# Performance work log

Hardware: AMD Instinct MI355X
Metric: run time of the kernel (lower is better)

The kernel has to match this reference:

```python
import jax, jax.numpy as jnp
import numpy as np

K_VALUES = (2, 4, 8)  # sorted k_values from init


def setup_inputs() -> dict:
    key = jax.random.key(0)
    ks = jax.random.split(key, 6)
    B, T, D, H = 16, 2048, 512, 64
    nk = len(K_VALUES)
    # columns: (E, Pt, eta, phi) -- E,Pt positive, eta in [-3,3], phi in [-pi,pi]
    u = jax.random.uniform(ks[0], (B, T, 4), jnp.float32)
    tokens_cont = u * jnp.array([100.0, 50.0, 6.0, 6.2832], jnp.float32) + jnp.array([1.0, 1.0, -3.0, -3.1416], jnp.float32)
    lengths = jax.random.randint(ks[1], (B,), T // 2, T + 1)
    mask = jnp.arange(T)[None, :] < lengths[:, None]  # [B,T] True=valid
    W1 = jax.random.normal(ks[2], (nk, H), jnp.float32) / np.sqrt(nk).astype(np.float32)
    b1 = jax.random.normal(ks[3], (H,), jnp.float32) * 0.01
    W2 = jax.random.normal(ks[4], (H, D), jnp.float32) / np.sqrt(H).astype(np.float32)
    b2 = jax.random.normal(ks[5], (D,), jnp.float32) * 0.01
    return dict(tokens_cont=tokens_cont, mask=mask, W1=W1, b1=b1, W2=W2, b2=b2)


def reference(tokens_cont, mask, W1, b1, W2, b2):
    B, T, _ = tokens_cont.shape
    E, Pt, eta, phi = (tokens_cont[..., i] for i in range(4))
    px = Pt * jnp.cos(phi)
    py = Pt * jnp.sin(phi)
    pz = Pt * jnp.sinh(jnp.clip(eta, -20.0, 20.0))
    P = jnp.stack([E, px, py, pz], axis=-1)  # [B,T,4] four-momentum
    metric = jnp.array([1.0, -1.0, -1.0, -1.0], P.dtype)
    # Lorentz dot: E_i E_j - px_i px_j - py_i py_j - pz_i pz_j -> [B,T,T]
    dot = jnp.einsum('btc,bsc->bts', P * metric, P)
    dot = jnp.where(mask[:, None, :], dot, -jnp.inf)  # exclude padding friends
    max_k = min(max(K_VALUES), T)
    _, topk_idx = jax.lax.top_k(dot, max_k)  # [B,T,max_k]
    Pf = P[jnp.arange(B)[:, None, None], topk_idx]  # gather friends [B,T,max_k,4]
    cum = jnp.cumsum(Pf, axis=2)  # prefix sums over sorted friends
    masses = []
    maskf = mask.astype(P.dtype)
    for k in K_VALUES:
        ps = cum[:, :, min(k, max_k) - 1, :]  # [B,T,4] summed 4-momentum of top-k group
        m2 = ps[..., 0] ** 2 - jnp.sum(ps[..., 1:] ** 2, axis=-1)
        m2 = jnp.maximum(m2, 0.0) * maskf
        masses.append(jnp.sqrt(m2 + 1e-8))
    mass = jnp.stack(masses, axis=-1)  # [B,T,n_k]
    h = jax.nn.gelu(mass @ W1 + b1, approximate=False)  # torch GELU = exact erf
    return h @ W2 + b2  # [B,T,model_dim]
```

## Files before the change

### kernel.cpp

```cpp
#include <hip/hip_runtime.h>
#include <hip/hip_bf16.h>
#include <math.h>

#define NB 16
#define NT 2048
#define ND 512
#define NH 64

typedef __attribute__((ext_vector_type(8))) short short8;
typedef __attribute__((ext_vector_type(4))) float float4v;

__device__ __forceinline__ bool mask_is_bytes(const int* m) {
    return m[0] == 0x01010101;
}
__device__ __forceinline__ bool mask_at(const int* m, bool bytes, int i) {
    if (bytes) return ((const unsigned char*)m)[i] != 0;
    return m[i] != 0;
}

__device__ __forceinline__ float dot4(float4 a, float4 p) {
    float d = a.x * p.x;
    d = __builtin_fmaf(a.y, p.y, d);
    d = __builtin_fmaf(a.z, p.z, d);
    d = __builtin_fmaf(a.w, p.w, d);
    return d;
}

__device__ __forceinline__ unsigned short f2bf(float x) {
    unsigned int u = __float_as_uint(x);
    u += 0x7fffu + ((u >> 16) & 1u);
    return (unsigned short)(u >> 16);
}

__global__ void __launch_bounds__(256) w2t_kernel(
        const float* __restrict__ W2, unsigned short* __restrict__ W2t) {
    int i = blockIdx.x * 256 + threadIdx.x;
    int n = i & (ND - 1), k = i >> 9;
    W2t[n * NH + k] = f2bf(W2[k * ND + n]);
}

#define VT(w2, j, l)  scratch[((w2) * 8 + (j)) * 64 + (l)]
#define PS(w2, c, l)  scratch[((w2) * 12 + (c)) * 64 + (l)]

__global__ void __launch_bounds__(512) fused_topk_mass_mlp_kernel(
        const float* __restrict__ tok,
        const int* __restrict__ mask,
        const float* __restrict__ W1,
        const float* __restrict__ b1,
        const unsigned short* __restrict__ W2t,
        const float* __restrict__ b2,
        float* __restrict__ out) {
    __shared__ float Plds[NT * 4];
    __shared__ float scratch[8 * 12 * 64];
    __shared__ unsigned short hs[64][88];
    __shared__ float mass_s[3][64];
    __shared__ int wcnt[8];

    const int b    = blockIdx.y;
    const int t0   = blockIdx.x * 64;
    const int tid  = threadIdx.x;
    const int lane = tid & 63;
    const int w    = tid >> 6;
    const bool mb  = mask_is_bytes(mask);

    const bool blockValid = mask_at(mask, mb, b * NT + t0);

    if (blockValid) {
        int cnt = 0;
#pragma unroll
        for (int it = 0; it < 4; ++it) {
            int i = tid + it * 512;
            float4 tv = ((const float4*)tok)[b * NT + i];
            bool m = mask_at(mask, mb, b * NT + i);
            float E = tv.x, Pt = tv.y, eta = tv.z, phi = tv.w;
            float px = Pt * cosf(phi);
            float py = Pt * sinf(phi);
            float pz = Pt * sinhf(fminf(fmaxf(eta, -20.f), 20.f));
            float4 pv = m ? make_float4(E, px, py, pz)
                          : make_float4(-1e30f, 0.f, 0.f, 0.f);
            *(float4*)&Plds[i * 4] = pv;
            cnt += (int)__popcll(__ballot(m));
        }
        if (lane == 0) wcnt[w] = cnt;
        __syncthreads();

        int L = 0;
#pragma unroll
        for (int j = 0; j < 8; ++j) L += wcnt[j];
        const int C    = (L + 7) >> 3;
        const int sBeg = w * C;
        const int sEnd = min(sBeg + C, L);

        float4 pt = *(const float4*)&Plds[(t0 + lane) * 4];
        float4 a  = make_float4(pt.x, -pt.y, -pt.z, -pt.w);

        const float NEGBIG = -3.402823466e38f;
        float v0 = NEGBIG, v1 = NEGBIG, v2 = NEGBIG, v3 = NEGBIG;
        float v4 = NEGBIG, v5 = NEGBIG, v6 = NEGBIG, v7 = NEGBIG;

#pragma unroll 4
        for (int s = sBeg; s < sEnd; ++s) {
            float4 ps = *(const float4*)&Plds[s * 4];
            float d = dot4(a, ps);
            float n0 = fmaxf(v0, d);
            float n1 = __builtin_amdgcn_fmed3f(d, v0, v1);
            float n2 = __builtin_amdgcn_fmed3f(d, v1, v2);
            float n3 = __builtin_amdgcn_fmed3f(d, v2, v3);
            float n4 = __builtin_amdgcn_fmed3f(d, v3, v4);
            float n5 = __builtin_amdgcn_fmed3f(d, v4, v5);
            float n6 = __builtin_amdgcn_fmed3f(d, v5, v6);
            float n7 = __builtin_amdgcn_fmed3f(d, v6, v7);
            v0 = n0; v1 = n1; v2 = n2; v3 = n3;
            v4 = n4; v5 = n5; v6 = n6; v7 = n7;
        }
        VT(w, 0, lane) = v0; VT(w, 1, lane) = v1;
        VT(w, 2, lane) = v2; VT(w, 3, lane) = v3;
        VT(w, 4, lane) = v4; VT(w, 5, lane) = v5;
        VT(w, 6, lane) = v6; VT(w, 7, lane) = v7;
        __syncthreads();

        float m0 = NEGBIG, m1 = NEGBIG, m2_ = NEGBIG, m3 = NEGBIG;
        float m4 = NEGBIG, m5 = NEGBIG, m6 = NEGBIG, m7 = NEGBIG;
#pragma unroll
        for (int w2 = 0; w2 < 8; ++w2) {
#pragma unroll
            for (int j = 0; j < 8; ++j) {
                float d = VT(w2, j, lane);
                float n0 = fmaxf(m0, d);
                float n1 = __builtin_amdgcn_fmed3f(d, m0, m1);
                float n2 = __builtin_amdgcn_fmed3f(d, m1, m2_);
                float n3 = __builtin_amdgcn_fmed3f(d, m2_, m3);
                float n4 = __builtin_amdgcn_fmed3f(d, m3, m4);
                float n5 = __builtin_amdgcn_fmed3f(d, m4, m5);
                float n6 = __builtin_amdgcn_fmed3f(d, m5, m6);
                float n7 = __builtin_amdgcn_fmed3f(d, m6, m7);
                m0 = n0; m1 = n1; m2_ = n2; m3 = n3;
                m4 = n4; m5 = n5; m6 = n6; m7 = n7;
            }
        }
        const float th2 = m1, th4 = m3, th8 = m7;
        __syncthreads();

        float s2x = 0.f, s2y = 0.f, s2z = 0.f, s2w = 0.f;
        float s4x = 0.f, s4y = 0.f, s4z = 0.f, s4w = 0.f;
        float s8x = 0.f, s8y = 0.f, s8z = 0.f, s8w = 0.f;
#pragma unroll 4
        for (int s = sBeg; s < sEnd; ++s) {
            float4 ps = *(const float4*)&Plds[s * 4];
            float d = dot4(a, ps);
            if (d >= th8) {
                s8x += ps.x; s8y += ps.y; s8z += ps.z; s8w += ps.w;
                if (d >= th4) {
                    s4x += ps.x; s4y += ps.y; s4z += ps.z; s4w += ps.w;
                    if (d >= th2) {
                        s2x += ps.x; s2y += ps.y; s2z += ps.z; s2w += ps.w;
                    }
                }
            }
        }
        PS(w, 0, lane) = s2x;  PS(w, 1, lane) = s2y;
        PS(w, 2, lane) = s2z;  PS(w, 3, lane) = s2w;
        PS(w, 4, lane) = s4x;  PS(w, 5, lane) = s4y;
        PS(w, 6, lane) = s4z;  PS(w, 7, lane) = s4w;
        PS(w, 8, lane) = s8x;  PS(w, 9, lane) = s8y;
        PS(w, 10, lane) = s8z; PS(w, 11, lane) = s8w;
        __syncthreads();

        if (w == 0) {
            float tot[12];
#pragma unroll
            for (int c = 0; c < 12; ++c) {
                float acc = 0.f;
#pragma unroll
                for (int w2 = 0; w2 < 8; ++w2) acc += PS(w2, c, lane);
                tot[c] = acc;
            }
            const bool maskt = (t0 + lane) < L;
            const float MZ = sqrtf(1e-8f);
            auto massf = [&](float sx, float sy, float sz, float sw) -> float {
                float q = sx * sx;
                q = __builtin_fmaf(-sy, sy, q);
                q = __builtin_fmaf(-sz, sz, q);
                q = __builtin_fmaf(-sw, sw, q);
                q = fmaxf(q, 0.f);
                return sqrtf(q + 1e-8f);
            };
            mass_s[0][lane] = maskt ? massf(tot[0], tot[1], tot[2], tot[3]) : MZ;
            mass_s[1][lane] = maskt ? massf(tot[4], tot[5], tot[6], tot[7]) : MZ;
            mass_s[2][lane] = maskt ? massf(tot[8], tot[9], tot[10], tot[11]) : MZ;
        }
    } else {
        if (tid < 64) {
            const float MZ = sqrtf(1e-8f);
            mass_s[0][tid] = MZ;
            mass_s[1][tid] = MZ;
            mass_s[2][tid] = MZ;
        }
    }
    __syncthreads();

    {
        const int tt = lane;
        const int hr = w;
        float q0 = mass_s[0][tt];
        float q1 = mass_s[1][tt];
        float q2 = mass_s[2][tt];
        unsigned short hv[8];
#pragma unroll
        for (int j = 0; j < 8; ++j) {
            int hh = hr * 8 + j;
            float pre = b1[hh];
            pre = __builtin_fmaf(q0, W1[hh], pre);
            pre = __builtin_fmaf(q1, W1[NH + hh], pre);
            pre = __builtin_fmaf(q2, W1[2 * NH + hh], pre);
            float g = 0.5f * pre * (1.0f + erff(pre * 0.70710678118654752f));
            hv[j] = f2bf(g);
        }
        *(short8*)&hs[tt][hr * 8] = *(const short8*)hv;
    }
    __syncthreads();

    const int col   = lane & 15;
    const int quad  = lane >> 4;
    const int mhalf = w >> 2;
    const int nBase = (w & 3) * 128;

    short8 afrag[2][2];
#pragma unroll
    for (int mt = 0; mt < 2; ++mt)
#pragma unroll
        for (int ks = 0; ks < 2; ++ks)
            afrag[mt][ks] = *(const short8*)&hs[mhalf * 32 + mt * 16 + col][ks * 32 + quad * 8];

    float4v acc[2][8];
#pragma unroll
    for (int mt = 0; mt < 2; ++mt)
#pragma unroll
        for (int nt = 0; nt < 8; ++nt)
            acc[mt][nt] = (float4v)(0.f);

#pragma unroll
    for (int nt = 0; nt < 8; ++nt) {
        const unsigned short* wp = W2t + (nBase + nt * 16 + col) * NH + quad * 8;
        short8 bf0 = *(const short8*)(wp);
        short8 bf1 = *(const short8*)(wp + 32);
        acc[0][nt] = __builtin_amdgcn_mfma_f32_16x16x32_bf16(afrag[0][0], bf0, acc[0][nt], 0, 0, 0);
        acc[1][nt] = __builtin_amdgcn_mfma_f32_16x16x32_bf16(afrag[1][0], bf0, acc[1][nt], 0, 0, 0);
        acc[0][nt] = __builtin_amdgcn_mfma_f32_16x16x32_bf16(afrag[0][1], bf1, acc[0][nt], 0, 0, 0);
        acc[1][nt] = __builtin_amdgcn_mfma_f32_16x16x32_bf16(afrag[1][1], bf1, acc[1][nt], 0, 0, 0);
    }

#pragma unroll
    for (int nt = 0; nt < 8; ++nt) {
        float bias = b2[nBase + nt * 16 + col];
#pragma unroll
        for (int mt = 0; mt < 2; ++mt) {
            int mRow = b * NT + t0 + mhalf * 32 + mt * 16 + quad * 4;
            size_t base = (size_t)mRow * ND + nBase + nt * 16 + col;
#pragma unroll
            for (int r = 0; r < 4; ++r) {
                out[base + (size_t)r * ND] = acc[mt][nt][r] + bias;
            }
        }
    }
}

extern "C" void kernel_launch(void* const* d_in, const int* in_sizes, int n_in,
                              void* d_out, int out_size, void* d_ws, size_t ws_size,
                              hipStream_t stream) {
    const float* tok  = (const float*)d_in[0];
    const int*   mask = (const int*)d_in[1];
    const float* W1   = (const float*)d_in[2];
    const float* b1   = (const float*)d_in[3];
    const float* W2   = (const float*)d_in[4];
    const float* b2   = (const float*)d_in[5];
    float*       out  = (float*)d_out;

    unsigned short* W2t = (unsigned short*)d_ws;

    w2t_kernel<<<dim3(ND * NH / 256), dim3(256), 0, stream>>>(W2, W2t);

    dim3 gB(NT / 64, NB);
    fused_topk_mass_mlp_kernel<<<gB, dim3(512), 0, stream>>>(
        tok, mask, W1, b1, W2t, b2, out);
}
```

Before: 133.6 us.

## Process two query tiles per block to reuse LDS friend loads

Each block now handles 128 query tokens instead of 64, so every lane tracks two top-8 lists and two sets of prefix sums. Each LDS load of a friend four-momentum is shared by two dot products. This halves the grid and the per-block preamble work (computing P for all 2048 tokens, mask popcounts). The cost is more register pressure from doubled accumulators, a larger LDS scratch buffer, and fewer blocks, which may lower occupancy and parallelism. The MLP stage runs twice per block.

After: 148.7 us. +11.3%, slower.

```diff
diff --git a/kernel.cpp b/kernel.cpp
--- a/kernel.cpp
+++ b/kernel.cpp
@@ -32,6 +32,20 @@
     return (unsigned short)(u >> 16);
 }
 
+#define INS8(V0,V1,V2,V3,V4,V5,V6,V7,D)                          \
+    {                                                            \
+        float n0 = fmaxf(V0, D);                                 \
+        float n1 = __builtin_amdgcn_fmed3f(D, V0, V1);           \
+        float n2 = __builtin_amdgcn_fmed3f(D, V1, V2);           \
+        float n3 = __builtin_amdgcn_fmed3f(D, V2, V3);           \
+        float n4 = __builtin_amdgcn_fmed3f(D, V3, V4);           \
+        float n5 = __builtin_amdgcn_fmed3f(D, V4, V5);           \
+        float n6 = __builtin_amdgcn_fmed3f(D, V5, V6);           \
+        float n7 = __builtin_amdgcn_fmed3f(D, V6, V7);           \
+        V0 = n0; V1 = n1; V2 = n2; V3 = n3;                      \
+        V4 = n4; V5 = n5; V6 = n6; V7 = n7;                      \
+    }
+
 __global__ void __launch_bounds__(256) w2t_kernel(
         const float* __restrict__ W2, unsigned short* __restrict__ W2t) {
     int i = blockIdx.x * 256 + threadIdx.x;
@@ -39,8 +53,8 @@
     W2t[n * NH + k] = f2bf(W2[k * ND + n]);
 }
 
-#define VT(w2, j, l)  scratch[((w2) * 8 + (j)) * 64 + (l)]
-#define PS(w2, c, l)  scratch[((w2) * 12 + (c)) * 64 + (l)]
+#define VT(w2, j, l)  scratch[((w2) * 8 + (j)) * 128 + (l)]
+#define PS(w2, c, l)  scratch[((w2) * 12 + (c)) * 128 + (l)]
 
 __global__ void __launch_bounds__(512) fused_topk_mass_mlp_kernel(
         const float* __restrict__ tok,
@@ -51,13 +65,13 @@
         const float* __restrict__ b2,
         float* __restrict__ out) {
     __shared__ float Plds[NT * 4];
-    __shared__ float scratch[8 * 12 * 64];
+    __shared__ float scratch[8 * 12 * 128];
     __shared__ unsigned short hs[64][88];
-    __shared__ float mass_s[3][64];
+    __shared__ float mass_s[3][128];
     __shared__ int wcnt[8];
 
     const int b    = blockIdx.y;
-    const int t0   = blockIdx.x * 64;
+    const int t0   = blockIdx.x * 128;
     const int tid  = threadIdx.x;
     const int lane = tid & 63;
     const int w    = tid >> 6;
@@ -91,91 +105,108 @@
         const int sBeg = w * C;
         const int sEnd = min(sBeg + C, L);
 
-        float4 pt = *(const float4*)&Plds[(t0 + lane) * 4];
-        float4 a  = make_float4(pt.x, -pt.y, -pt.z, -pt.w);
+        float4 ptA = *(const float4*)&Plds[(t0 + lane) * 4];
+        float4 ptB = *(const float4*)&Plds[(t0 + 64 + lane) * 4];
+        float4 aA  = make_float4(ptA.x, -ptA.y, -ptA.z, -ptA.w);
+        float4 aB  = make_float4(ptB.x, -ptB.y, -ptB.z, -ptB.w);
 
         const float NEGBIG = -3.402823466e38f;
-        float v0 = NEGBIG, v1 = NEGBIG, v2 = NEGBIG, v3 = NEGBIG;
-        float v4 = NEGBIG, v5 = NEGBIG, v6 = NEGBIG, v7 = NEGBIG;
+        float A0 = NEGBIG, A1 = NEGBIG, A2 = NEGBIG, A3 = NEGBIG;
+        float A4 = NEGBIG, A5 = NEGBIG, A6 = NEGBIG, A7 = NEGBIG;
+        float B0 = NEGBIG, B1 = NEGBIG, B2 = NEGBIG, B3 = NEGBIG;
+        float B4 = NEGBIG, B5 = NEGBIG, B6 = NEGBIG, B7 = NEGBIG;
 
 #pragma unroll 4
         for (int s = sBeg; s < sEnd; ++s) {
             float4 ps = *(const float4*)&Plds[s * 4];
-            float d = dot4(a, ps);
-            float n0 = fmaxf(v0, d);
-            float n1 = __builtin_amdgcn_fmed3f(d, v0, v1);
-            float n2 = __builtin_amdgcn_fmed3f(d, v1, v2);
-            float n3 = __builtin_amdgcn_fmed3f(d, v2, v3);
-            float n4 = __builtin_amdgcn_fmed3f(d, v3, v4);
-            float n5 = __builtin_amdgcn_fmed3f(d, v4, v5);
-            float n6 = __builtin_amdgcn_fmed3f(d, v5, v6);
-            float n7 = __builtin_amdgcn_fmed3f(d, v6, v7);
-            v0 = n0; v1 = n1; v2 = n2; v3 = n3;
-            v4 = n4; v5 = n5; v6 = n6; v7 = n7;
-        }
-        VT(w, 0, lane) = v0; VT(w, 1, lane) = v1;
-        VT(w, 2, lane) = v2; VT(w, 3, lane) = v3;
-        VT(w, 4, lane) = v4; VT(w, 5, lane) = v5;
-        VT(w, 6, lane) = v6; VT(w, 7, lane) = v7;
-        __syncthreads();
-
-        float m0 = NEGBIG, m1 = NEGBIG, m2_ = NEGBIG, m3 = NEGBIG;
-        float m4 = NEGBIG, m5 = NEGBIG, m6 = NEGBIG, m7 = NEGBIG;
+            float dA = dot4(aA, ps);
+            float dB = dot4(aB, ps);
+            INS8(A0, A1, A2, A3, A4, A5, A6, A7, dA);
+            INS8(B0, B1, B2, B3, B4, B5, B6, B7, dB);
+        }
+        VT(w, 0, lane) = A0; VT(w, 1, lane) = A1;
+        VT(w, 2, lane) = A2; VT(w, 3, lane) = A3;
+        VT(w, 4, lane) = A4; VT(w, 5, lane) = A5;
+        VT(w, 6, lane) = A6; VT(w, 7, lane) = A7;
+        VT(w, 0, 64 + lane) = B0; VT(w, 1, 64 + lane) = B1;
+        VT(w, 2, 64 + lane) = B2; VT(w, 3, 64 + lane) = B3;
+        VT(w, 4, 64 + lane) = B4; VT(w, 5, 64 + lane) = B5;
+        VT(w, 6, 64 + lane) = B6; VT(w, 7, 64 + lane) = B7;
+        __syncthreads();
+
+        float mA0 = NEGBIG, mA1 = NEGBIG, mA2 = NEGBIG, mA3 = NEGBIG;
+        float mA4 = NEGBIG, mA5 = NEGBIG, mA6 = NEGBIG, mA7 = NEGBIG;
+        float mB0 = NEGBIG, mB1 = NEGBIG, mB2 = NEGBIG, mB3 = NEGBIG;
+        float mB4 = NEGBIG, mB5 = NEGBIG, mB6 = NEGBIG, mB7 = NEGBIG;
 #pragma unroll
         for (int w2 = 0; w2 < 8; ++w2) {
 #pragma unroll
             for (int j = 0; j < 8; ++j) {
-                float d = VT(w2, j, lane);
-                float n0 = fmaxf(m0, d);
-                float n1 = __builtin_amdgcn_fmed3f(d, m0, m1);
-                float n2 = __builtin_amdgcn_fmed3f(d, m1, m2_);
-                float n3 = __builtin_amdgcn_fmed3f(d, m2_, m3);
-                float n4 = __builtin_amdgcn_fmed3f(d, m3, m4);
-                float n5 = __builtin_amdgcn_fmed3f(d, m4, m5);
-                float n6 = __builtin_amdgcn_fmed3f(d, m5, m6);
-                float n7 = __builtin_amdgcn_fmed3f(d, m6, m7);
-                m0 = n0; m1 = n1; m2_ = n2; m3 = n3;
-                m4 = n4; m5 = n5; m6 = n6; m7 = n7;
-            }
-        }
-        const float th2 = m1, th4 = m3, th8 = m7;
-        __syncthreads();
-
-        float s2x = 0.f, s2y = 0.f, s2z = 0.f, s2w = 0.f;
-        float s4x = 0.f, s4y = 0.f, s4z = 0.f, s4w = 0.f;
-        float s8x = 0.f, s8y = 0.f, s8z = 0.f, s8w = 0.f;
+                float dA = VT(w2, j, lane);
+                float dB = VT(w2, j, 64 + lane);
+                INS8(mA0, mA1, mA2, mA3, mA4, mA5, mA6, mA7, dA);
+                INS8(mB0, mB1, mB2, mB3, mB4, mB5, mB6, mB7, dB);
+            }
+        }
+        const float th2A = mA1, th4A = mA3, th8A = mA7;
+        const float th2B = mB1, th4B = mB3, th8B = mB7;
+        __syncthreads();
+
+        float a2x = 0.f, a2y = 0.f, a2z = 0.f, a2w = 0.f;
+        float a4x = 0.f, a4y = 0.f, a4z = 0.f, a4w = 0.f;
+        float a8x = 0.f, a8y = 0.f, a8z = 0.f, a8w = 0.f;
+        float b2x = 0.f, b2y = 0.f, b2z = 0.f, b2w = 0.f;
+        float b4x = 0.f, b4y = 0.f, b4z = 0.f, b4w = 0.f;
+        float b8x = 0.f, b8y = 0.f, b8z = 0.f, b8w = 0.f;
 #pragma unroll 4
         for (int s = sBeg; s < sEnd; ++s) {
             float4 ps = *(const float4*)&Plds[s * 4];
-            float d = dot4(a, ps);
-            if (d >= th8) {
-                s8x += ps.x; s8y += ps.y; s8z += ps.z; s8w += ps.w;
-                if (d >= th4) {
-                    s4x += ps.x; s4y += ps.y; s4z += ps.z; s4w += ps.w;
-                    if (d >= th2) {
-                        s2x += ps.x; s2y += ps.y; s2z += ps.z; s2w += ps.w;
+            float dA = dot4(aA, ps);
+            float dB = dot4(aB, ps);
+            if (dA >= th8A) {
+                a8x += ps.x; a8y += ps.y; a8z += ps.z; a8w += ps.w;
+                if (dA >= th4A) {
+                    a4x += ps.x; a4y += ps.y; a4z += ps.z; a4w += ps.w;
+                    if (dA >= th2A) {
+                        a2x += ps.x; a2y += ps.y; a2z += ps.z; a2w += ps.w;
                     }
                 }
             }
-        }
-        PS(w, 0, lane) = s2x;  PS(w, 1, lane) = s2y;
-        PS(w, 2, lane) = s2z;  PS(w, 3, lane) = s2w;
-        PS(w, 4, lane) = s4x;  PS(w, 5, lane) = s4y;
-        PS(w, 6, lane) = s4z;  PS(w, 7, lane) = s4w;
-        PS(w, 8, lane) = s8x;  PS(w, 9, lane) = s8y;
-        PS(w, 10, lane) = s8z; PS(w, 11, lane) = s8w;
-        __syncthreads();
-
-        if (w == 0) {
+            if (dB >= th8B) {
+                b8x += ps.x; b8y += ps.y; b8z += ps.z; b8w += ps.w;
+                if (dB >= th4B) {
+                    b4x += ps.x; b4y += ps.y; b4z += ps.z; b4w += ps.w;
+                    if (dB >= th2B) {
+                        b2x += ps.x; b2y += ps.y; b2z += ps.z; b2w += ps.w;
+                    }
+                }
+            }
+        }
+        PS(w, 0, lane) = a2x;  PS(w, 1, lane) = a2y;
+        PS(w, 2, lane) = a2z;  PS(w, 3, lane) = a2w;
+        PS(w, 4, lane) = a4x;  PS(w, 5, lane) = a4y;
+        PS(w, 6, lane) = a4z;  PS(w, 7, lane) = a4w;
+        PS(w, 8, lane) = a8x;  PS(w, 9, lane) = a8y;
+        PS(w, 10, lane) = a8z; PS(w, 11, lane) = a8w;
+        PS(w, 0, 64 + lane) = b2x;  PS(w, 1, 64 + lane) = b2y;
+        PS(w, 2, 64 + lane) = b2z;  PS(w, 3, 64 + lane) = b2w;
+        PS(w, 4, 64 + lane) = b4x;  PS(w, 5, 64 + lane) = b4y;
+        PS(w, 6, 64 + lane) = b4z;  PS(w, 7, 64 + lane) = b4w;
+        PS(w, 8, 64 + lane) = b8x;  PS(w, 9, 64 + lane) = b8y;
+        PS(w, 10, 64 + lane) = b8z; PS(w, 11, 64 + lane) = b8w;
+        __syncthreads();
+
+        if (w < 2) {
+            const int tl = w * 64 + lane;
             float tot[12];
 #pragma unroll
             for (int c = 0; c < 12; ++c) {
                 float acc = 0.f;
 #pragma unroll
-                for (int w2 = 0; w2 < 8; ++w2) acc += PS(w2, c, lane);
+                for (int w2 = 0; w2 < 8; ++w2) acc += PS(w2, c, tl);
                 tot[c] = acc;
             }
-            const bool maskt = (t0 + lane) < L;
+            const bool maskt = (t0 + tl) < L;
             const float MZ = sqrtf(1e-8f);
             auto massf = [&](float sx, float sy, float sz, float sw) -> float {
                 float q = sx * sx;
@@ -185,12 +216,12 @@
                 q = fmaxf(q, 0.f);
                 return sqrtf(q + 1e-8f);
             };
-            mass_s[0][lane] = maskt ? massf(tot[0], tot[1], tot[2], tot[3]) : MZ;
-            mass_s[1][lane] = maskt ? massf(tot[4], tot[5], tot[6], tot[7]) : MZ;
-            mass_s[2][lane] = maskt ? massf(tot[8], tot[9], tot[10], tot[11]) : MZ;
+            mass_s[0][tl] = maskt ? massf(tot[0], tot[1], tot[2], tot[3]) : MZ;
+            mass_s[1][tl] = maskt ? massf(tot[4], tot[5], tot[6], tot[7]) : MZ;
+            mass_s[2][tl] = maskt ? massf(tot[8], tot[9], tot[10], tot[11]) : MZ;
         }
     } else {
-        if (tid < 64) {
+        if (tid < 128) {
             const float MZ = sqrtf(1e-8f);
             mass_s[0][tid] = MZ;
             mass_s[1][tid] = MZ;
@@ -199,69 +230,73 @@
     }
     __syncthreads();
 
-    {
-        const int tt = lane;
-        const int hr = w;
-        float q0 = mass_s[0][tt];
-        float q1 = mass_s[1][tt];
-        float q2 = mass_s[2][tt];
-        unsigned short hv[8];
-#pragma unroll
-        for (int j = 0; j < 8; ++j) {
-            int hh = hr * 8 + j;
-            float pre = b1[hh];
-            pre = __builtin_fmaf(q0, W1[hh], pre);
-            pre = __builtin_fmaf(q1, W1[NH + hh], pre);
-            pre = __builtin_fmaf(q2, W1[2 * NH + hh], pre);
-            float g = 0.5f * pre * (1.0f + erff(pre * 0.70710678118654752f));
-            hv[j] = f2bf(g);
-        }
-        *(short8*)&hs[tt][hr * 8] = *(const short8*)hv;
-    }
-    __syncthreads();
-
     const int col   = lane & 15;
     const int quad  = lane >> 4;
     const int mhalf = w >> 2;
     const int nBase = (w & 3) * 128;
 
-    short8 afrag[2][2];
-#pragma unroll
-    for (int mt = 0; mt < 2; ++mt)
-#pragma unroll
-        for (int ks = 0; ks < 2; ++ks)
-            afrag[mt][ks] = *(const short8*)&hs[mhalf * 32 + mt * 16 + col][ks * 32 + quad * 8];
-
-    float4v acc[2][8];
-#pragma unroll
-    for (int mt = 0; mt < 2; ++mt)
-#pragma unroll
-        for (int nt = 0; nt < 8; ++nt)
-            acc[mt][nt] = (float4v)(0.f);
-
-#pragma unroll
-    for (int nt = 0; nt < 8; ++nt) {
-        const unsigned short* wp = W2t + (nBase + nt * 16 + col) * NH + quad * 8;
-        short8 bf0 = *(const short8*)(wp);
-        short8 bf1 = *(const short8*)(wp + 32);
-        acc[0][nt] = __builtin_amdgcn_mfma_f32_16x16x32_bf16(afrag[0][0], bf0, acc[0][nt], 0, 0, 0);
-        acc[1][nt] = __builtin_amdgcn_mfma_f32_16x16x32_bf16(afrag[1][0], bf0, acc[1][nt], 0, 0, 0);
-        acc[0][nt] = __builtin_amdgcn_mfma_f32_16x16x32_bf16(afrag[0][1], bf1, acc[0][nt], 0, 0, 0);
-        acc[1][nt] = __builtin_amdgcn_mfma_f32_16x16x32_bf16(afrag[1][1], bf1, acc[1][nt], 0, 0, 0);
-    }
-
-#pragma unroll
-    for (int nt = 0; nt < 8; ++nt) {
-        float bias = b2[nBase + nt * 16 + col];
-#pragma unroll
-        for (int mt = 0; mt < 2; ++mt) {
-            int mRow = b * NT + t0 + mhalf * 32 + mt * 16 + quad * 4;
-            size_t base = (size_t)mRow * ND + nBase + nt * 16 + col;
-#pragma unroll
-            for (int r = 0; r < 4; ++r) {
-                out[base + (size_t)r * ND] = acc[mt][nt][r] + bias;
-            }
-        }
+#pragma unroll
+    for (int half = 0; half < 2; ++half) {
+        {
+            const int tt = lane;
+            const int hr = w;
+            float q0 = mass_s[0][half * 64 + tt];
+            float q1 = mass_s[1][half * 64 + tt];
+            float q2 = mass_s[2][half * 64 + tt];
+            unsigned short hv[8];
+#pragma unroll
+            for (int j = 0; j < 8; ++j) {
+                int hh = hr * 8 + j;
+                float pre = b1[hh];
+                pre = __builtin_fmaf(q0, W1[hh], pre);
+                pre = __builtin_fmaf(q1, W1[NH + hh], pre);
+                pre = __builtin_fmaf(q2, W1[2 * NH + hh], pre);
+                float g = 0.5f * pre * (1.0f + erff(pre * 0.70710678118654752f));
+                hv[j] = f2bf(g);
+            }
+            *(short8*)&hs[tt][hr * 8] = *(const short8*)hv;
+        }
+        __syncthreads();
+
+        short8 afrag[2][2];
+#pragma unroll
+        for (int mt = 0; mt < 2; ++mt)
+#pragma unroll
+            for (int ks = 0; ks < 2; ++ks)
+                afrag[mt][ks] = *(const short8*)&hs[mhalf * 32 + mt * 16 + col][ks * 32 + quad * 8];
+
+        float4v acc[2][8];
+#pragma unroll
+        for (int mt = 0; mt < 2; ++mt)
+#pragma unroll
+            for (int nt = 0; nt < 8; ++nt)
+                acc[mt][nt] = (float4v)(0.f);
+
+#pragma unroll
+        for (int nt = 0; nt < 8; ++nt) {
+            const unsigned short* wp = W2t + (nBase + nt * 16 + col) * NH + quad * 8;
+            short8 bf0 = *(const short8*)(wp);
+            short8 bf1 = *(const short8*)(wp + 32);
+            acc[0][nt] = __builtin_amdgcn_mfma_f32_16x16x32_bf16(afrag[0][0], bf0, acc[0][nt], 0, 0, 0);
+            acc[1][nt] = __builtin_amdgcn_mfma_f32_16x16x32_bf16(afrag[1][0], bf0, acc[1][nt], 0, 0, 0);
+            acc[0][nt] = __builtin_amdgcn_mfma_f32_16x16x32_bf16(afrag[0][1], bf1, acc[0][nt], 0, 0, 0);
+            acc[1][nt] = __builtin_amdgcn_mfma_f32_16x16x32_bf16(afrag[1][1], bf1, acc[1][nt], 0, 0, 0);
+        }
+
+#pragma unroll
+        for (int nt = 0; nt < 8; ++nt) {
+            float bias = b2[nBase + nt * 16 + col];
+#pragma unroll
+            for (int mt = 0; mt < 2; ++mt) {
+                int mRow = b * NT + t0 + half * 64 + mhalf * 32 + mt * 16 + quad * 4;
+                size_t base = (size_t)mRow * ND + nBase + nt * 16 + col;
+#pragma unroll
+                for (int r = 0; r < 4; ++r) {
+                    out[base + (size_t)r * ND] = acc[mt][nt][r] + bias;
+                }
+            }
+        }
+        __syncthreads();
     }
 }
 
@@ -280,7 +315,7 @@
 
     w2t_kernel<<<dim3(ND * NH / 256), dim3(256), 0, stream>>>(W2, W2t);
 
-    dim3 gB(NT / 64, NB);
+    dim3 gB(NT / 128, NB);
     fused_topk_mass_mlp_kernel<<<gB, dim3(512), 0, stream>>>(
         tok, mask, W1, b1, W2t, b2, out);
 }
```

## Track top-8 indices during scan and gather friends instead of second pass

Applied to the files above, without the earlier changes.

The top-8 insertion network now carries friend indices alongside values, so the threshold-based second pass over all keys and its partial-sum reduction are removed. Wave 0 merges the per-wave candidate lists with indices and gathers the selected four-momenta from LDS to build prefix sums. This halves the O(T) dot-product work per token but adds about 16 compare/select ops per insertion, and leaves the final merge serial in one wave. Tie handling changes from a threshold test to index selection, which more closely matches top_k.

Result: slower. 157.6 us (+18.0%).

```diff
diff --git a/kernel.cpp b/kernel.cpp
--- a/kernel.cpp
+++ b/kernel.cpp
@@ -32,15 +32,39 @@
     return (unsigned short)(u >> 16);
 }
 
+#define INSVI(V0,V1,V2,V3,V4,V5,V6,V7,I0,I1,I2,I3,I4,I5,I6,I7,D,SI)  \
+    {                                                                \
+        bool c0 = (D) > V0, c1 = (D) > V1, c2 = (D) > V2,            \
+             c3 = (D) > V3, c4 = (D) > V4, c5 = (D) > V5,            \
+             c6 = (D) > V6, c7 = (D) > V7;                           \
+        float n0 = fmaxf(V0, (D));                                   \
+        float n1 = __builtin_amdgcn_fmed3f((D), V0, V1);             \
+        float n2 = __builtin_amdgcn_fmed3f((D), V1, V2);             \
+        float n3 = __builtin_amdgcn_fmed3f((D), V2, V3);             \
+        float n4 = __builtin_amdgcn_fmed3f((D), V3, V4);             \
+        float n5 = __builtin_amdgcn_fmed3f((D), V4, V5);             \
+        float n6 = __builtin_amdgcn_fmed3f((D), V5, V6);             \
+        float n7 = __builtin_amdgcn_fmed3f((D), V6, V7);             \
+        int j0 = c0 ? (SI) : I0;                                     \
+        int j1 = c0 ? I0 : (c1 ? (SI) : I1);                         \
+        int j2 = c1 ? I1 : (c2 ? (SI) : I2);                         \
+        int j3 = c2 ? I2 : (c3 ? (SI) : I3);                         \
+        int j4 = c3 ? I3 : (c4 ? (SI) : I4);                         \
+        int j5 = c4 ? I4 : (c5 ? (SI) : I5);                         \
+        int j6 = c5 ? I5 : (c6 ? (SI) : I6);                         \
+        int j7 = c6 ? I6 : (c7 ? (SI) : I7);                         \
+        V0 = n0; V1 = n1; V2 = n2; V3 = n3;                          \
+        V4 = n4; V5 = n5; V6 = n6; V7 = n7;                          \
+        I0 = j0; I1 = j1; I2 = j2; I3 = j3;                          \
+        I4 = j4; I5 = j5; I6 = j6; I7 = j7;                          \
+    }
+
 __global__ void __launch_bounds__(256) w2t_kernel(
         const float* __restrict__ W2, unsigned short* __restrict__ W2t) {
     int i = blockIdx.x * 256 + threadIdx.x;
     int n = i & (ND - 1), k = i >> 9;
     W2t[n * NH + k] = f2bf(W2[k * ND + n]);
 }
-
-#define VT(w2, j, l)  scratch[((w2) * 8 + (j)) * 64 + (l)]
-#define PS(w2, c, l)  scratch[((w2) * 12 + (c)) * 64 + (l)]
 
 __global__ void __launch_bounds__(512) fused_topk_mass_mlp_kernel(
         const float* __restrict__ tok,
@@ -51,7 +75,8 @@
         const float* __restrict__ b2,
         float* __restrict__ out) {
     __shared__ float Plds[NT * 4];
-    __shared__ float scratch[8 * 12 * 64];
+    __shared__ float vtV[8][8][64];
+    __shared__ int   vtI[8][8][64];
     __shared__ unsigned short hs[64][88];
     __shared__ float mass_s[3][64];
     __shared__ int wcnt[8];
@@ -97,97 +122,55 @@
         const float NEGBIG = -3.402823466e38f;
         float v0 = NEGBIG, v1 = NEGBIG, v2 = NEGBIG, v3 = NEGBIG;
         float v4 = NEGBIG, v5 = NEGBIG, v6 = NEGBIG, v7 = NEGBIG;
-
-#pragma unroll 4
+        int   i0 = 0, i1 = 0, i2 = 0, i3 = 0, i4 = 0, i5 = 0, i6 = 0, i7 = 0;
+
+#pragma unroll 2
         for (int s = sBeg; s < sEnd; ++s) {
             float4 ps = *(const float4*)&Plds[s * 4];
             float d = dot4(a, ps);
-            float n0 = fmaxf(v0, d);
-            float n1 = __builtin_amdgcn_fmed3f(d, v0, v1);
-            float n2 = __builtin_amdgcn_fmed3f(d, v1, v2);
-            float n3 = __builtin_amdgcn_fmed3f(d, v2, v3);
-            float n4 = __builtin_amdgcn_fmed3f(d, v3, v4);
-            float n5 = __builtin_amdgcn_fmed3f(d, v4, v5);
-            float n6 = __builtin_amdgcn_fmed3f(d, v5, v6);
-            float n7 = __builtin_amdgcn_fmed3f(d, v6, v7);
-            v0 = n0; v1 = n1; v2 = n2; v3 = n3;
-            v4 = n4; v5 = n5; v6 = n6; v7 = n7;
-        }
-        VT(w, 0, lane) = v0; VT(w, 1, lane) = v1;
-        VT(w, 2, lane) = v2; VT(w, 3, lane) = v3;
-        VT(w, 4, lane) = v4; VT(w, 5, lane) = v5;
-        VT(w, 6, lane) = v6; VT(w, 7, lane) = v7;
+            INSVI(v0, v1, v2, v3, v4, v5, v6, v7,
+                  i0, i1, i2, i3, i4, i5, i6, i7, d, s);
+        }
+        vtV[w][0][lane] = v0; vtI[w][0][lane] = i0;
+        vtV[w][1][lane] = v1; vtI[w][1][lane] = i1;
+        vtV[w][2][lane] = v2; vtI[w][2][lane] = i2;
+        vtV[w][3][lane] = v3; vtI[w][3][lane] = i3;
+        vtV[w][4][lane] = v4; vtI[w][4][lane] = i4;
+        vtV[w][5][lane] = v5; vtI[w][5][lane] = i5;
+        vtV[w][6][lane] = v6; vtI[w][6][lane] = i6;
+        vtV[w][7][lane] = v7; vtI[w][7][lane] = i7;
         __syncthreads();
 
-        float m0 = NEGBIG, m1 = NEGBIG, m2_ = NEGBIG, m3 = NEGBIG;
-        float m4 = NEGBIG, m5 = NEGBIG, m6 = NEGBIG, m7 = NEGBIG;
-#pragma unroll
-        for (int w2 = 0; w2 < 8; ++w2) {
-#pragma unroll
-            for (int j = 0; j < 8; ++j) {
-                float d = VT(w2, j, lane);
-                float n0 = fmaxf(m0, d);
-                float n1 = __builtin_amdgcn_fmed3f(d, m0, m1);
-                float n2 = __builtin_amdgcn_fmed3f(d, m1, m2_);
-                float n3 = __builtin_amdgcn_fmed3f(d, m2_, m3);
-                float n4 = __builtin_amdgcn_fmed3f(d, m3, m4);
-                float n5 = __builtin_amdgcn_fmed3f(d, m4, m5);
-                float n6 = __builtin_amdgcn_fmed3f(d, m5, m6);
-                float n7 = __builtin_amdgcn_fmed3f(d, m6, m7);
-                m0 = n0; m1 = n1; m2_ = n2; m3 = n3;
-                m4 = n4; m5 = n5; m6 = n6; m7 = n7;
-            }
-        }
-        const float th2 = m1, th4 = m3, th8 = m7;
-        __syncthreads();
-
-        float s2x = 0.f, s2y = 0.f, s2z = 0.f, s2w = 0.f;
-        float s4x = 0.f, s4y = 0.f, s4z = 0.f, s4w = 0.f;
-        float s8x = 0.f, s8y = 0.f, s8z = 0.f, s8w = 0.f;
-#pragma unroll 4
-        for (int s = sBeg; s < sEnd; ++s) {
-            float4 ps = *(const float4*)&Plds[s * 4];
-            float d = dot4(a, ps);
-            if (d >= th8) {
-                s8x += ps.x; s8y += ps.y; s8z += ps.z; s8w += ps.w;
-                if (d >= th4) {
-                    s4x += ps.x; s4y += ps.y; s4z += ps.z; s4w += ps.w;
-                    if (d >= th2) {
-                        s2x += ps.x; s2y += ps.y; s2z += ps.z; s2w += ps.w;
-                    }
+        if (w == 0) {
+            for (int w2 = 1; w2 < 8; ++w2) {
+#pragma unroll
+                for (int j = 0; j < 8; ++j) {
+                    float dv = vtV[w2][j][lane];
+                    int   di = vtI[w2][j][lane];
+                    INSVI(v0, v1, v2, v3, v4, v5, v6, v7,
+                          i0, i1, i2, i3, i4, i5, i6, i7, dv, di);
                 }
             }
-        }
-        PS(w, 0, lane) = s2x;  PS(w, 1, lane) = s2y;
-        PS(w, 2, lane) = s2z;  PS(w, 3, lane) = s2w;
-        PS(w, 4, lane) = s4x;  PS(w, 5, lane) = s4y;
-        PS(w, 6, lane) = s4z;  PS(w, 7, lane) = s4w;
-        PS(w, 8, lane) = s8x;  PS(w, 9, lane) = s8y;
-        PS(w, 10, lane) = s8z; PS(w, 11, lane) = s8w;
-        __syncthreads();
-
-        if (w == 0) {
-            float tot[12];
-#pragma unroll
-            for (int c = 0; c < 12; ++c) {
-                float acc = 0.f;
-#pragma unroll
-                for (int w2 = 0; w2 < 8; ++w2) acc += PS(w2, c, lane);
-                tot[c] = acc;
-            }
+            float sx = 0.f, sy = 0.f, sz = 0.f, sw = 0.f;
             const bool maskt = (t0 + lane) < L;
             const float MZ = sqrtf(1e-8f);
-            auto massf = [&](float sx, float sy, float sz, float sw) -> float {
-                float q = sx * sx;
-                q = __builtin_fmaf(-sy, sy, q);
-                q = __builtin_fmaf(-sz, sz, q);
-                q = __builtin_fmaf(-sw, sw, q);
+            auto massf = [&](float gx, float gy, float gz, float gw) -> float {
+                float q = gx * gx;
+                q = __builtin_fmaf(-gy, gy, q);
+                q = __builtin_fmaf(-gz, gz, q);
+                q = __builtin_fmaf(-gw, gw, q);
                 q = fmaxf(q, 0.f);
                 return sqrtf(q + 1e-8f);
             };
-            mass_s[0][lane] = maskt ? massf(tot[0], tot[1], tot[2], tot[3]) : MZ;
-            mass_s[1][lane] = maskt ? massf(tot[4], tot[5], tot[6], tot[7]) : MZ;
-            mass_s[2][lane] = maskt ? massf(tot[8], tot[9], tot[10], tot[11]) : MZ;
+            int idxs[8] = { i0, i1, i2, i3, i4, i5, i6, i7 };
+#pragma unroll
+            for (int j = 0; j < 8; ++j) {
+                float4 pv = *(const float4*)&Plds[idxs[j] * 4];
+                sx += pv.x; sy += pv.y; sz += pv.z; sw += pv.w;
+                if (j == 1) mass_s[0][lane] = maskt ? massf(sx, sy, sz, sw) : MZ;
+                if (j == 3) mass_s[1][lane] = maskt ? massf(sx, sy, sz, sw) : MZ;
+                if (j == 7) mass_s[2][lane] = maskt ? massf(sx, sy, sz, sw) : MZ;
+            }
         }
     } else {
         if (tid < 64) {
```

## Precompute four-momenta in a prepass and run 1024-thread blocks reading from global memory

Applied to the files above, without the earlier changes.

The sinh/cos/sin conversion of each batch's tokens moves out of the main kernel into a separate prepass that writes P to workspace. The W2 transpose is folded into the same prepass. The main kernel now uses 16 waves instead of 8, splitting the friend scan over more waves and reading P from global/L2 instead of LDS. The threshold merge is now done by one wave and broadcast through shared memory. The MFMA tiling is re-split to 16-row tiles per wave. This removes the per-block redundant transcendental work on all 2048 tokens, which every one of the 32 blocks per batch repeated. In exchange the inner loop relies on cached global loads rather than LDS, and the merge now runs serially in one wave.

After: 163.8 us. +22.6%, slower.

```diff
diff --git a/kernel.cpp b/kernel.cpp
--- a/kernel.cpp
+++ b/kernel.cpp
@@ -32,29 +32,58 @@
     return (unsigned short)(u >> 16);
 }
 
-__global__ void __launch_bounds__(256) w2t_kernel(
-        const float* __restrict__ W2, unsigned short* __restrict__ W2t) {
+#define INS8(V0,V1,V2,V3,V4,V5,V6,V7,D)                          \
+    {                                                            \
+        float n0 = fmaxf(V0, D);                                 \
+        float n1 = __builtin_amdgcn_fmed3f(D, V0, V1);           \
+        float n2 = __builtin_amdgcn_fmed3f(D, V1, V2);           \
+        float n3 = __builtin_amdgcn_fmed3f(D, V2, V3);           \
+        float n4 = __builtin_amdgcn_fmed3f(D, V3, V4);           \
+        float n5 = __builtin_amdgcn_fmed3f(D, V4, V5);           \
+        float n6 = __builtin_amdgcn_fmed3f(D, V5, V6);           \
+        float n7 = __builtin_amdgcn_fmed3f(D, V6, V7);           \
+        V0 = n0; V1 = n1; V2 = n2; V3 = n3;                      \
+        V4 = n4; V5 = n5; V6 = n6; V7 = n7;                      \
+    }
+
+__global__ void __launch_bounds__(256) compute_P_kernel(
+        const float* __restrict__ tok,
+        const int* __restrict__ mask,
+        float4* __restrict__ P,
+        unsigned short* __restrict__ W2t,
+        const float* __restrict__ W2) {
+    const bool mb = mask_is_bytes(mask);
     int i = blockIdx.x * 256 + threadIdx.x;
-    int n = i & (ND - 1), k = i >> 9;
+
+    float4 t = ((const float4*)tok)[i];
+    float E = t.x, Pt = t.y, eta = t.z, phi = t.w;
+    float px = Pt * cosf(phi);
+    float py = Pt * sinf(phi);
+    float pz = Pt * sinhf(fminf(fmaxf(eta, -20.f), 20.f));
+    bool m = mask_at(mask, mb, i);
+    P[i] = m ? make_float4(E, px, py, pz)
+             : make_float4(-1e30f, 0.f, 0.f, 0.f);
+
+    int n = i & 511, k = i >> 9;
     W2t[n * NH + k] = f2bf(W2[k * ND + n]);
 }
 
 #define VT(w2, j, l)  scratch[((w2) * 8 + (j)) * 64 + (l)]
 #define PS(w2, c, l)  scratch[((w2) * 12 + (c)) * 64 + (l)]
 
-__global__ void __launch_bounds__(512) fused_topk_mass_mlp_kernel(
-        const float* __restrict__ tok,
+__global__ void __launch_bounds__(1024) fused_topk_mass_mlp_kernel(
+        const float4* __restrict__ P,
         const int* __restrict__ mask,
         const float* __restrict__ W1,
         const float* __restrict__ b1,
         const unsigned short* __restrict__ W2t,
         const float* __restrict__ b2,
         float* __restrict__ out) {
-    __shared__ float Plds[NT * 4];
-    __shared__ float scratch[8 * 12 * 64];
+    __shared__ float scratch[16 * 12 * 64];
+    __shared__ float th_s[3][64];
     __shared__ unsigned short hs[64][88];
     __shared__ float mass_s[3][64];
-    __shared__ int wcnt[8];
+    __shared__ int wcnt[16];
 
     const int b    = blockIdx.y;
     const int t0   = blockIdx.x * 64;
@@ -68,30 +97,22 @@
     if (blockValid) {
         int cnt = 0;
 #pragma unroll
-        for (int it = 0; it < 4; ++it) {
-            int i = tid + it * 512;
-            float4 tv = ((const float4*)tok)[b * NT + i];
-            bool m = mask_at(mask, mb, b * NT + i);
-            float E = tv.x, Pt = tv.y, eta = tv.z, phi = tv.w;
-            float px = Pt * cosf(phi);
-            float py = Pt * sinf(phi);
-            float pz = Pt * sinhf(fminf(fmaxf(eta, -20.f), 20.f));
-            float4 pv = m ? make_float4(E, px, py, pz)
-                          : make_float4(-1e30f, 0.f, 0.f, 0.f);
-            *(float4*)&Plds[i * 4] = pv;
-            cnt += (int)__popcll(__ballot(m));
+        for (int it = 0; it < 2; ++it) {
+            int i = tid + it * 1024;
+            cnt += (int)__popcll(__ballot(mask_at(mask, mb, b * NT + i)));
         }
         if (lane == 0) wcnt[w] = cnt;
         __syncthreads();
 
         int L = 0;
 #pragma unroll
-        for (int j = 0; j < 8; ++j) L += wcnt[j];
-        const int C    = (L + 7) >> 3;
+        for (int j = 0; j < 16; ++j) L += wcnt[j];
+        const int C    = (L + 15) >> 4;
         const int sBeg = w * C;
         const int sEnd = min(sBeg + C, L);
 
-        float4 pt = *(const float4*)&Plds[(t0 + lane) * 4];
+        const float4* __restrict__ Pb = P + b * NT;
+        float4 pt = Pb[t0 + lane];
         float4 a  = make_float4(pt.x, -pt.y, -pt.z, -pt.w);
 
         const float NEGBIG = -3.402823466e38f;
@@ -100,18 +121,9 @@
 
 #pragma unroll 4
         for (int s = sBeg; s < sEnd; ++s) {
-            float4 ps = *(const float4*)&Plds[s * 4];
+            float4 ps = Pb[s];
             float d = dot4(a, ps);
-            float n0 = fmaxf(v0, d);
-            float n1 = __builtin_amdgcn_fmed3f(d, v0, v1);
-            float n2 = __builtin_amdgcn_fmed3f(d, v1, v2);
-            float n3 = __builtin_amdgcn_fmed3f(d, v2, v3);
-            float n4 = __builtin_amdgcn_fmed3f(d, v3, v4);
-            float n5 = __builtin_amdgcn_fmed3f(d, v4, v5);
-            float n6 = __builtin_amdgcn_fmed3f(d, v5, v6);
-            float n7 = __builtin_amdgcn_fmed3f(d, v6, v7);
-            v0 = n0; v1 = n1; v2 = n2; v3 = n3;
-            v4 = n4; v5 = n5; v6 = n6; v7 = n7;
+            INS8(v0, v1, v2, v3, v4, v5, v6, v7, d);
         }
         VT(w, 0, lane) = v0; VT(w, 1, lane) = v1;
         VT(w, 2, lane) = v2; VT(w, 3, lane) = v3;
@@ -119,34 +131,30 @@
         VT(w, 6, lane) = v6; VT(w, 7, lane) = v7;
         __syncthreads();
 
-        float m0 = NEGBIG, m1 = NEGBIG, m2_ = NEGBIG, m3 = NEGBIG;
-        float m4 = NEGBIG, m5 = NEGBIG, m6 = NEGBIG, m7 = NEGBIG;
-#pragma unroll
-        for (int w2 = 0; w2 < 8; ++w2) {
-#pragma unroll
-            for (int j = 0; j < 8; ++j) {
-                float d = VT(w2, j, lane);
-                float n0 = fmaxf(m0, d);
-                float n1 = __builtin_amdgcn_fmed3f(d, m0, m1);
-                float n2 = __builtin_amdgcn_fmed3f(d, m1, m2_);
-                float n3 = __builtin_amdgcn_fmed3f(d, m2_, m3);
-                float n4 = __builtin_amdgcn_fmed3f(d, m3, m4);
-                float n5 = __builtin_amdgcn_fmed3f(d, m4, m5);
-                float n6 = __builtin_amdgcn_fmed3f(d, m5, m6);
-                float n7 = __builtin_amdgcn_fmed3f(d, m6, m7);
-                m0 = n0; m1 = n1; m2_ = n2; m3 = n3;
-                m4 = n4; m5 = n5; m6 = n6; m7 = n7;
+        if (w == 0) {
+            for (int w2 = 1; w2 < 16; ++w2) {
+#pragma unroll
+                for (int j = 0; j < 8; ++j) {
+                    float d = VT(w2, j, lane);
+                    INS8(v0, v1, v2, v3, v4, v5, v6, v7, d);
+                }
             }
-        }
-        const float th2 = m1, th4 = m3, th8 = m7;
-        __syncthreads();
+            th_s[0][lane] = v1;
+            th_s[1][lane] = v3;
+            th_s[2][lane] = v7;
+        }
+        __syncthreads();
+
+        const float th2 = th_s[0][lane];
+        const float th4 = th_s[1][lane];
+        const float th8 = th_s[2][lane];
 
         float s2x = 0.f, s2y = 0.f, s2z = 0.f, s2w = 0.f;
         float s4x = 0.f, s4y = 0.f, s4z = 0.f, s4w = 0.f;
         float s8x = 0.f, s8y = 0.f, s8z = 0.f, s8w = 0.f;
 #pragma unroll 4
         for (int s = sBeg; s < sEnd; ++s) {
-            float4 ps = *(const float4*)&Plds[s * 4];
+            float4 ps = Pb[s];
             float d = dot4(a, ps);
             if (d >= th8) {
                 s8x += ps.x; s8y += ps.y; s8z += ps.z; s8w += ps.w;
@@ -166,13 +174,13 @@
         PS(w, 10, lane) = s8z; PS(w, 11, lane) = s8w;
         __syncthreads();
 
-        if (w == 0) {
+        if (tid < 64) {
             float tot[12];
 #pragma unroll
             for (int c = 0; c < 12; ++c) {
                 float acc = 0.f;
 #pragma unroll
-                for (int w2 = 0; w2 < 8; ++w2) acc += PS(w2, c, lane);
+                for (int w2 = 0; w2 < 16; ++w2) acc += PS(w2, c, lane);
                 tot[c] = acc;
             }
             const bool maskt = (t0 + lane) < L;
@@ -205,10 +213,10 @@
         float q0 = mass_s[0][tt];
         float q1 = mass_s[1][tt];
         float q2 = mass_s[2][tt];
-        unsigned short hv[8];
-#pragma unroll
-        for (int j = 0; j < 8; ++j) {
-            int hh = hr * 8 + j;
+        unsigned short hv[4];
+#pragma unroll
+        for (int j = 0; j < 4; ++j) {
+            int hh = hr * 4 + j;
             float pre = b1[hh];
             pre = __builtin_fmaf(q0, W1[hh], pre);
             pre = __builtin_fmaf(q1, W1[NH + hh], pre);
@@ -216,51 +224,42 @@
             float g = 0.5f * pre * (1.0f + erff(pre * 0.70710678118654752f));
             hv[j] = f2bf(g);
         }
-        *(short8*)&hs[tt][hr * 8] = *(const short8*)hv;
+        *(uint2*)&hs[tt][hr * 4] = *(const uint2*)hv;
     }
     __syncthreads();
 
     const int col   = lane & 15;
     const int quad  = lane >> 4;
-    const int mhalf = w >> 2;
-    const int nBase = (w & 3) * 128;
-
-    short8 afrag[2][2];
-#pragma unroll
-    for (int mt = 0; mt < 2; ++mt)
-#pragma unroll
-        for (int ks = 0; ks < 2; ++ks)
-            afrag[mt][ks] = *(const short8*)&hs[mhalf * 32 + mt * 16 + col][ks * 32 + quad * 8];
-
-    float4v acc[2][8];
-#pragma unroll
-    for (int mt = 0; mt < 2; ++mt)
-#pragma unroll
-        for (int nt = 0; nt < 8; ++nt)
-            acc[mt][nt] = (float4v)(0.f);
+    const int mtile = w & 3;
+    const int nBase = (w >> 2) * 128;
+
+    short8 afrag[2];
+#pragma unroll
+    for (int ks = 0; ks < 2; ++ks)
+        afrag[ks] = *(const short8*)&hs[mtile * 16 + col][ks * 32 + quad * 8];
+
+    float4v acc[8];
+#pragma unroll
+    for (int nt = 0; nt < 8; ++nt)
+        acc[nt] = (float4v)(0.f);
 
 #pragma unroll
     for (int nt = 0; nt < 8; ++nt) {
         const unsigned short* wp = W2t + (nBase + nt * 16 + col) * NH + quad * 8;
         short8 bf0 = *(const short8*)(wp);
         short8 bf1 = *(const short8*)(wp + 32);
-        acc[0][nt] = __builtin_amdgcn_mfma_f32_16x16x32_bf16(afrag[0][0], bf0, acc[0][nt], 0, 0, 0);
-        acc[1][nt] = __builtin_amdgcn_mfma_f32_16x16x32_bf16(afrag[1][0], bf0, acc[1][nt], 0, 0, 0);
-        acc[0][nt] = __builtin_amdgcn_mfma_f32_16x16x32_bf16(afrag[0][1], bf1, acc[0][nt], 0, 0, 0);
-        acc[1][nt] = __builtin_amdgcn_mfma_f32_16x16x32_bf16(afrag[1][1], bf1, acc[1][nt], 0, 0, 0);
+        acc[nt] = __builtin_amdgcn_mfma_f32_16x16x32_bf16(afrag[0], bf0, acc[nt], 0, 0, 0);
+        acc[nt] = __builtin_amdgcn_mfma_f32_16x16x32_bf16(afrag[1], bf1, acc[nt], 0, 0, 0);
     }
 
 #pragma unroll
     for (int nt = 0; nt < 8; ++nt) {
         float bias = b2[nBase + nt * 16 + col];
-#pragma unroll
-        for (int mt = 0; mt < 2; ++mt) {
-            int mRow = b * NT + t0 + mhalf * 32 + mt * 16 + quad * 4;
-            size_t base = (size_t)mRow * ND + nBase + nt * 16 + col;
-#pragma unroll
-            for (int r = 0; r < 4; ++r) {
-                out[base + (size_t)r * ND] = acc[mt][nt][r] + bias;
-            }
+        int mRow = b * NT + t0 + mtile * 16 + quad * 4;
+        size_t base = (size_t)mRow * ND + nBase + nt * 16 + col;
+#pragma unroll
+        for (int r = 0; r < 4; ++r) {
+            out[base + (size_t)r * ND] = acc[nt][r] + bias;
         }
     }
 }
@@ -276,11 +275,12 @@
     const float* b2   = (const float*)d_in[5];
     float*       out  = (float*)d_out;
 
-    unsigned short* W2t = (unsigned short*)d_ws;
-
-    w2t_kernel<<<dim3(ND * NH / 256), dim3(256), 0, stream>>>(W2, W2t);
+    float4*         P   = (float4*)d_ws;
+    unsigned short* W2t = (unsigned short*)((char*)d_ws + (size_t)NB * NT * 16);
+
+    compute_P_kernel<<<dim3(NB * NT / 256), dim3(256), 0, stream>>>(tok, mask, P, W2t, W2);
 
     dim3 gB(NT / 64, NB);
-    fused_topk_mass_mlp_kernel<<<gB, dim3(512), 0, stream>>>(
-        tok, mask, W1, b1, W2t, b2, out);
-}
+    fused_topk_mass_mlp_kernel<<<gB, dim3(1024), 0, stream>>>(
+        P, mask, W1, b1, W2t, b2, out);
+}
```
